# Optimization experiments

Measured on AMD Instinct MI355X. Metric: run time of the kernel, lower is better.

## Reference

```python
import jax, jax.numpy as jnp
import numpy as np

B, Q, V, H, U = 4, 256, 2048, 512, 128

def setup_inputs() -> dict:
    key = jax.random.key(0)
    ks = jax.random.split(key, 5)
    return {
        "queries": jax.random.normal(ks[0], (B, Q, H), dtype=jnp.float32),
        "values": jax.random.normal(ks[1], (B, V, H), dtype=jnp.float32),
        "w1": jax.random.normal(ks[2], (H, U), dtype=jnp.float32) / np.sqrt(H),
        "w2": jax.random.normal(ks[3], (H, U), dtype=jnp.float32) / np.sqrt(H),
        "v": jax.random.normal(ks[4], (U,), dtype=jnp.float32) / np.sqrt(U),
    }

def reference(queries, values, w1, w2, v):
    # Project queries and values first (cheap GEMMs), then broadcast-add.
    pq = jnp.einsum("bqh,hu->bqu", queries, w1)          # [B,Q,U]
    pv = jnp.einsum("bvh,hu->bvu", values, w2)           # [B,V,U]
    # added_qv: [B,Q,V,U] -- the large intermediate the original materializes
    scores = jnp.einsum("bqvu,u->bqv", jnp.tanh(pq[:, :, None, :] + pv[:, None, :, :]), v)
    attn = jax.nn.softmax(scores, axis=-1)               # softmax over V (last axis, as tf.nn.softmax)
    return jnp.einsum("bqv,bvh->bqh", attn, values)      # [B,Q,H]
```

## Files before the change

### kernel.cpp

```cpp
#include <hip/hip_runtime.h>

#define BB 4
#define QQ 256
#define VV 2048
#define HH 512
#define UU 128

#define C2E   2.8853900817779268f
#define LOG2E 1.4426950408889634f

__device__ __forceinline__ void fma4(float4& a, float s, const float4& w) {
    a.x = fmaf(s, w.x, a.x);
    a.y = fmaf(s, w.y, a.y);
    a.z = fmaf(s, w.z, a.z);
    a.w = fmaf(s, w.w, a.w);
}
__device__ __forceinline__ float2 rcp2(float2 x) {
    return make_float2(__builtin_amdgcn_rcpf(x.x), __builtin_amdgcn_rcpf(x.y));
}
__device__ __forceinline__ float2 mul2(float2 a, float2 b) { return make_float2(a.x*b.x, a.y*b.y); }
__device__ __forceinline__ float2 muls(float2 a, float s)  { return make_float2(a.x*s, a.y*s); }
__device__ __forceinline__ float2 fma2(float2 a, float2 b, float2 c) {
    return make_float2(fmaf(a.x, b.x, c.x), fmaf(a.y, b.y, c.y));
}
__device__ __forceinline__ float2 fmas(float2 a, float s, float2 c) {
    return make_float2(fmaf(a.x, s, c.x), fmaf(a.y, s, c.y));
}

__global__ __launch_bounds__(256) void proj_kernel(const float* __restrict__ queries,
                                                   const float* __restrict__ values,
                                                   const float* __restrict__ w1,
                                                   const float* __restrict__ w2,
                                                   float* __restrict__ pqI,
                                                   float* __restrict__ pvI,
                                                   float* __restrict__ denom) {
    __shared__ float As[32][18];
    __shared__ float Ws[32 * 128];
    __shared__ float Ls[128][17];
    const int bid = blockIdx.x;
    const int tid = threadIdx.x;
    if (bid == 0) *(float4*)&denom[tid * 4] = make_float4(0.f, 0.f, 0.f, 0.f);

    const bool isv = (bid < 512);
    const float* A; const float* W; int b, r0, ROWS; float* Ob;
    if (isv) {
        b = bid >> 7; r0 = (bid & 127) * 16;
        A = values + ((size_t)(b * VV + r0)) * HH;  W = w2;
        Ob = pvI + (size_t)b * UU * VV;  ROWS = VV;
    } else {
        const int q = bid - 512;
        b = q >> 4; r0 = (q & 15) * 16;
        A = queries + ((size_t)(b * QQ + r0)) * HH; W = w1;
        Ob = pqI + (size_t)b * UU * QQ;  ROWS = QQ;
    }

    const int tx = tid & 31;
    const int ty = tid >> 5;
    float4 acc0 = make_float4(0.f, 0.f, 0.f, 0.f);
    float4 acc1 = make_float4(0.f, 0.f, 0.f, 0.f);

    for (int k0 = 0; k0 < HH; k0 += 32) {
        if (tid < 128) {
            const int r = tid >> 3, kk4 = (tid & 7) * 4;
            const float4 a = *(const float4*)&A[(size_t)r * HH + k0 + kk4];
            As[kk4 + 0][r] = a.x; As[kk4 + 1][r] = a.y;
            As[kk4 + 2][r] = a.z; As[kk4 + 3][r] = a.w;
        }
#pragma unroll
        for (int t = 0; t < 4; t++) {
            const int f = tid + t * 256;
            const int kk = f >> 5, u4 = (f & 31) * 4;
            *(float4*)&Ws[kk * 128 + u4] = *(const float4*)&W[(size_t)(k0 + kk) * UU + u4];
        }
        __syncthreads();
#pragma unroll
        for (int kk = 0; kk < 32; kk++) {
            const float2 a = *(const float2*)&As[kk][ty * 2];
            const float4 w = *(const float4*)&Ws[kk * 128 + tx * 4];
            fma4(acc0, a.x, w);
            fma4(acc1, a.y, w);
        }
        __syncthreads();
    }
    {
        const float a0[4] = {acc0.x, acc0.y, acc0.z, acc0.w};
        const float a1[4] = {acc1.x, acc1.y, acc1.z, acc1.w};
#pragma unroll
        for (int i = 0; i < 4; i++) {
            Ls[tx * 4 + i][ty * 2 + 0] = __builtin_amdgcn_exp2f(a0[i] * C2E);
            Ls[tx * 4 + i][ty * 2 + 1] = __builtin_amdgcn_exp2f(a1[i] * C2E);
        }
    }
    __syncthreads();
#pragma unroll
    for (int t = 0; t < 2; t++) {
        const int idx = tid + t * 256;
        const int g = idx >> 4, r = idx & 15;
        float4 o;
        o.x = Ls[4 * g + 0][r]; o.y = Ls[4 * g + 1][r];
        o.z = Ls[4 * g + 2][r]; o.w = Ls[4 * g + 3][r];
        *(float4*)&Ob[((size_t)g * ROWS + r0 + r) * 4] = o;
    }
}

__global__ __launch_bounds__(512, 6) void fused_kernel(const float* __restrict__ pqI,
                                                       const float* __restrict__ pvI,
                                                       const float* __restrict__ vvec,
                                                       const float* __restrict__ values,
                                                       float* __restrict__ slab,
                                                       float* __restrict__ denom) {
    __shared__ float att[256][8];
    __shared__ float scratch[8][512];
    __shared__ float wred[4][8];
    const int tid = threadIdx.x;
    const int bid = blockIdx.x;
    const int vs = bid & 7, qb = (bid >> 3) & 31, b = bid >> 8;
    const int qbase = qb * 8, vbase = vs * 256;

    const int vloc = tid & 255, uh = tid >> 8;
    const int v = vbase + vloc;

    float vsum = 0.0f;
#pragma unroll
    for (int u4 = 0; u4 < UU; u4 += 4) {
        const float4 t = *(const float4*)&vvec[u4];
        vsum += t.x + t.y + t.z + t.w;
    }

    const float* pv4 = pvI + (size_t)b * UU * VV + (size_t)v * 4;
    const float* pq4 = pqI + (size_t)b * UU * QQ + (size_t)qbase * 4;

    float2 acc[4];
#pragma unroll
    for (int p = 0; p < 4; p++) acc[p] = make_float2(0.f, 0.f);

    const int G0 = uh * 16;
    float4 ev = *(const float4*)&pv4[(size_t)G0 * VV * 4];

    for (int g = 0; g < 16; g++) {
        const int G = G0 + g;
        const float* eqp = &pq4[(size_t)G * QQ * 4];
        float4 eq[8];
#pragma unroll
        for (int qi = 0; qi < 8; qi++) eq[qi] = *(const float4*)&eqp[qi * 4];
        float4 evn;
        if (g < 15) evn = *(const float4*)&pv4[(size_t)(G + 1) * VV * 4];
        const float4 wq = *(const float4*)&vvec[G * 4];
        const float w0 = 2.f * wq.x, w1 = 2.f * wq.y;
        const float w2 = 2.f * wq.z, w3 = 2.f * wq.w;
#pragma unroll
        for (int p = 0; p < 4; p++) {
            const float4 e0 = eq[2 * p], e1 = eq[2 * p + 1];
            const float2 a1 = make_float2(fmaf(e0.x, ev.x, 1.f), fmaf(e1.x, ev.x, 1.f));
            const float2 b1 = make_float2(fmaf(e0.y, ev.y, 1.f), fmaf(e1.y, ev.y, 1.f));
            const float2 c1 = make_float2(fmaf(e0.z, ev.z, 1.f), fmaf(e1.z, ev.z, 1.f));
            const float2 d1 = make_float2(fmaf(e0.w, ev.w, 1.f), fmaf(e1.w, ev.w, 1.f));
            const float2 pab = mul2(a1, b1), pcd = mul2(c1, d1);
            const float2 nab = fmas(a1, w1, muls(b1, w0));
            const float2 ncd = fmas(c1, w3, muls(d1, w2));
            const float2 num = fma2(nab, pcd, mul2(ncd, pab));
            const float2 den = mul2(pab, pcd);
            acc[p] = fma2(num, rcp2(den), acc[p]);
        }
        ev = evn;
    }

    float* cbuf = &scratch[0][0];
    if (uh == 1) {
#pragma unroll
        for (int p = 0; p < 4; p++)
            *(float2*)&cbuf[vloc * 8 + 2 * p] = acc[p];
    }
    __syncthreads();
    if (uh == 0) {
#pragma unroll
        for (int p = 0; p < 4; p++) {
            const float2 hi = *(const float2*)&cbuf[vloc * 8 + 2 * p];
            float2 e;
            e.x = __builtin_amdgcn_exp2f((vsum - (acc[p].x + hi.x)) * LOG2E);
            e.y = __builtin_amdgcn_exp2f((vsum - (acc[p].y + hi.y)) * LOG2E);
            att[vloc][2 * p + 0] = e.x;
            att[vloc][2 * p + 1] = e.y;
            acc[p] = e;
        }
#pragma unroll
        for (int off = 1; off < 64; off <<= 1) {
#pragma unroll
            for (int p = 0; p < 4; p++) {
                acc[p].x += __shfl_xor(acc[p].x, off, 64);
                acc[p].y += __shfl_xor(acc[p].y, off, 64);
            }
        }
        if ((tid & 63) == 0) {
            const int w = tid >> 6;
#pragma unroll
            for (int p = 0; p < 4; p++) {
                wred[w][2 * p + 0] = acc[p].x;
                wred[w][2 * p + 1] = acc[p].y;
            }
        }
    }
    __syncthreads();
    if (tid < 8)
        atomicAdd(&denom[b * QQ + qbase + tid],
                  wred[0][tid] + wred[1][tid] + wred[2][tid] + wred[3][tid]);

    const int hg = tid & 127, sel = tid >> 7;
    const int qh = sel & 1, vh = sel >> 1;
    const int h0 = hg * 4;
    const float* vp = values + ((size_t)(b * VV + vbase + vh * 128)) * HH + h0;

    float4 oacc[4];
#pragma unroll
    for (int j = 0; j < 4; j++) oacc[j] = make_float4(0.f, 0.f, 0.f, 0.f);

#pragma unroll 2
    for (int vv = 0; vv < 128; vv++) {
        const float4 w = *(const float4*)&vp[(size_t)vv * HH];
        const float4 a = *(const float4*)&att[vh * 128 + vv][qh * 4];
        fma4(oacc[0], a.x, w); fma4(oacc[1], a.y, w);
        fma4(oacc[2], a.z, w); fma4(oacc[3], a.w, w);
    }

    if (vh == 1) {
#pragma unroll
        for (int j = 0; j < 4; j++) *(float4*)&scratch[qh * 4 + j][h0] = oacc[j];
    }
    __syncthreads();
    if (vh == 0) {
        float* sp = slab + (size_t)vs * (BB * QQ * HH);
#pragma unroll
        for (int j = 0; j < 4; j++) {
            const float4 p4 = *(const float4*)&scratch[qh * 4 + j][h0];
            const int q = qh * 4 + j;
            float4 o;
            o.x = oacc[j].x + p4.x; o.y = oacc[j].y + p4.y;
            o.z = oacc[j].z + p4.z; o.w = oacc[j].w + p4.w;
            *(float4*)&sp[((size_t)(b * QQ + qbase + q)) * HH + h0] = o;
        }
    }
}

__global__ __launch_bounds__(256) void reduce_kernel(const float* __restrict__ slab,
                                                     const float* __restrict__ denom,
                                                     float* __restrict__ out) {
    const int i = blockIdx.x * 256 + threadIdx.x;
    const float r = __builtin_amdgcn_rcpf(denom[i >> 7]);
    const float4* s4 = (const float4*)slab;
    float4 s = s4[i];
#pragma unroll
    for (int k = 1; k < 8; k++) {
        const float4 p = s4[(size_t)k * (BB * QQ * HH / 4) + i];
        s.x += p.x; s.y += p.y; s.z += p.z; s.w += p.w;
    }
    s.x *= r; s.y *= r; s.z *= r; s.w *= r;
    ((float4*)out)[i] = s;
}

extern "C" void kernel_launch(void* const* d_in, const int* in_sizes, int n_in,
                              void* d_out, int out_size, void* d_ws, size_t ws_size,
                              hipStream_t stream) {
    const float* queries = (const float*)d_in[0];
    const float* values  = (const float*)d_in[1];
    const float* w1      = (const float*)d_in[2];
    const float* w2      = (const float*)d_in[3];
    const float* vvec    = (const float*)d_in[4];
    float* out = (float*)d_out;

    float* ws    = (float*)d_ws;
    float* pqI   = ws;
    float* pvI   = pqI + BB * UU * QQ;
    float* denom = pvI + (size_t)BB * UU * VV;
    float* slab  = denom + BB * QQ;

    proj_kernel<<<512 + 64, 256, 0, stream>>>(queries, values, w1, w2, pqI, pvI, denom);
    fused_kernel<<<BB * (QQ / 8) * (VV / 256), 512, 0, stream>>>(pqI, pvI, vvec, values, slab, denom);
    reduce_kernel<<<(BB * QQ * HH) / 4 / 256, 256, 0, stream>>>(slab, denom, out);
}
```

Before: 189.5 us.

## Double per-block query tile in fused and projection kernels for more reuse

The fused kernel now handles 16 queries per block instead of 8, so each pv element and each values row loaded in the attention-weighted sum is reused across twice as many queries, and the grid halves to 512 blocks. The projection kernel computes 32 rows per block with a 4x4 register tile and shares one LDS buffer between the A/W tiles and the transpose buffer. Register pressure in the fused kernel rises (8 float2 plus 8 float4 accumulators under a 512x6 launch bound), so spills or lower occupancy are a risk, and the smaller grid may leave some CUs less busy.

Measured after the change: 173.3 us. -8.5%, faster.

```diff
diff --git a/kernel.cpp b/kernel.cpp
--- a/kernel.cpp
+++ b/kernel.cpp
@@ -34,33 +34,36 @@
                                                    float* __restrict__ pqI,
                                                    float* __restrict__ pvI,
                                                    float* __restrict__ denom) {
-    __shared__ float As[32][18];
-    __shared__ float Ws[32 * 128];
-    __shared__ float Ls[128][17];
+    __shared__ float smem[32 * 36 + 32 * 128];
+    float (*As)[36] = (float(*)[36])smem;
+    float* Ws = smem + 32 * 36;
+    float (*Ls)[36] = (float(*)[36])smem;
+
     const int bid = blockIdx.x;
     const int tid = threadIdx.x;
     if (bid == 0) *(float4*)&denom[tid * 4] = make_float4(0.f, 0.f, 0.f, 0.f);
 
-    const bool isv = (bid < 512);
+    const bool isv = (bid < 256);
     const float* A; const float* W; int b, r0, ROWS; float* Ob;
     if (isv) {
-        b = bid >> 7; r0 = (bid & 127) * 16;
+        b = bid >> 6; r0 = (bid & 63) * 32;
         A = values + ((size_t)(b * VV + r0)) * HH;  W = w2;
         Ob = pvI + (size_t)b * UU * VV;  ROWS = VV;
     } else {
-        const int q = bid - 512;
-        b = q >> 4; r0 = (q & 15) * 16;
+        const int q = bid - 256;
+        b = q >> 3; r0 = (q & 7) * 32;
         A = queries + ((size_t)(b * QQ + r0)) * HH; W = w1;
         Ob = pqI + (size_t)b * UU * QQ;  ROWS = QQ;
     }
 
     const int tx = tid & 31;
     const int ty = tid >> 5;
-    float4 acc0 = make_float4(0.f, 0.f, 0.f, 0.f);
-    float4 acc1 = make_float4(0.f, 0.f, 0.f, 0.f);
+    float4 acc[4];
+#pragma unroll
+    for (int j = 0; j < 4; j++) acc[j] = make_float4(0.f, 0.f, 0.f, 0.f);
 
     for (int k0 = 0; k0 < HH; k0 += 32) {
-        if (tid < 128) {
+        {
             const int r = tid >> 3, kk4 = (tid & 7) * 4;
             const float4 a = *(const float4*)&A[(size_t)r * HH + k0 + kk4];
             As[kk4 + 0][r] = a.x; As[kk4 + 1][r] = a.y;
@@ -75,27 +78,27 @@
         __syncthreads();
 #pragma unroll
         for (int kk = 0; kk < 32; kk++) {
-            const float2 a = *(const float2*)&As[kk][ty * 2];
+            const float4 a = *(const float4*)&As[kk][ty * 4];
             const float4 w = *(const float4*)&Ws[kk * 128 + tx * 4];
-            fma4(acc0, a.x, w);
-            fma4(acc1, a.y, w);
+            fma4(acc[0], a.x, w);
+            fma4(acc[1], a.y, w);
+            fma4(acc[2], a.z, w);
+            fma4(acc[3], a.w, w);
         }
         __syncthreads();
     }
-    {
-        const float a0[4] = {acc0.x, acc0.y, acc0.z, acc0.w};
-        const float a1[4] = {acc1.x, acc1.y, acc1.z, acc1.w};
-#pragma unroll
-        for (int i = 0; i < 4; i++) {
-            Ls[tx * 4 + i][ty * 2 + 0] = __builtin_amdgcn_exp2f(a0[i] * C2E);
-            Ls[tx * 4 + i][ty * 2 + 1] = __builtin_amdgcn_exp2f(a1[i] * C2E);
-        }
-    }
-    __syncthreads();
-#pragma unroll
-    for (int t = 0; t < 2; t++) {
+#pragma unroll
+    for (int j = 0; j < 4; j++) {
+        const float aa[4] = {acc[j].x, acc[j].y, acc[j].z, acc[j].w};
+#pragma unroll
+        for (int i = 0; i < 4; i++)
+            Ls[tx * 4 + i][ty * 4 + j] = __builtin_amdgcn_exp2f(aa[i] * C2E);
+    }
+    __syncthreads();
+#pragma unroll
+    for (int t = 0; t < 4; t++) {
         const int idx = tid + t * 256;
-        const int g = idx >> 4, r = idx & 15;
+        const int g = idx >> 5, r = idx & 31;
         float4 o;
         o.x = Ls[4 * g + 0][r]; o.y = Ls[4 * g + 1][r];
         o.z = Ls[4 * g + 2][r]; o.w = Ls[4 * g + 3][r];
@@ -109,13 +112,13 @@
                                                        const float* __restrict__ values,
                                                        float* __restrict__ slab,
                                                        float* __restrict__ denom) {
-    __shared__ float att[256][8];
-    __shared__ float scratch[8][512];
-    __shared__ float wred[4][8];
+    __shared__ float att[256][16];
+    __shared__ float scratch[16][512];
+    __shared__ float wred[4][16];
     const int tid = threadIdx.x;
     const int bid = blockIdx.x;
-    const int vs = bid & 7, qb = (bid >> 3) & 31, b = bid >> 8;
-    const int qbase = qb * 8, vbase = vs * 256;
+    const int vs = bid & 7, qb = (bid >> 3) & 15, b = bid >> 7;
+    const int qbase = qb * 16, vbase = vs * 256;
 
     const int vloc = tid & 255, uh = tid >> 8;
     const int v = vbase + vloc;
@@ -130,9 +133,9 @@
     const float* pv4 = pvI + (size_t)b * UU * VV + (size_t)v * 4;
     const float* pq4 = pqI + (size_t)b * UU * QQ + (size_t)qbase * 4;
 
-    float2 acc[4];
-#pragma unroll
-    for (int p = 0; p < 4; p++) acc[p] = make_float2(0.f, 0.f);
+    float2 acc[8];
+#pragma unroll
+    for (int p = 0; p < 8; p++) acc[p] = make_float2(0.f, 0.f);
 
     const int G0 = uh * 16;
     float4 ev = *(const float4*)&pv4[(size_t)G0 * VV * 4];
@@ -140,17 +143,15 @@
     for (int g = 0; g < 16; g++) {
         const int G = G0 + g;
         const float* eqp = &pq4[(size_t)G * QQ * 4];
-        float4 eq[8];
-#pragma unroll
-        for (int qi = 0; qi < 8; qi++) eq[qi] = *(const float4*)&eqp[qi * 4];
         float4 evn;
         if (g < 15) evn = *(const float4*)&pv4[(size_t)(G + 1) * VV * 4];
         const float4 wq = *(const float4*)&vvec[G * 4];
         const float w0 = 2.f * wq.x, w1 = 2.f * wq.y;
         const float w2 = 2.f * wq.z, w3 = 2.f * wq.w;
 #pragma unroll
-        for (int p = 0; p < 4; p++) {
-            const float4 e0 = eq[2 * p], e1 = eq[2 * p + 1];
+        for (int p = 0; p < 8; p++) {
+            const float4 e0 = *(const float4*)&eqp[(2 * p) * 4];
+            const float4 e1 = *(const float4*)&eqp[(2 * p + 1) * 4];
             const float2 a1 = make_float2(fmaf(e0.x, ev.x, 1.f), fmaf(e1.x, ev.x, 1.f));
             const float2 b1 = make_float2(fmaf(e0.y, ev.y, 1.f), fmaf(e1.y, ev.y, 1.f));
             const float2 c1 = make_float2(fmaf(e0.z, ev.z, 1.f), fmaf(e1.z, ev.z, 1.f));
@@ -168,14 +169,14 @@
     float* cbuf = &scratch[0][0];
     if (uh == 1) {
 #pragma unroll
-        for (int p = 0; p < 4; p++)
-            *(float2*)&cbuf[vloc * 8 + 2 * p] = acc[p];
+        for (int p = 0; p < 8; p++)
+            *(float2*)&cbuf[vloc * 16 + 2 * p] = acc[p];
     }
     __syncthreads();
     if (uh == 0) {
 #pragma unroll
-        for (int p = 0; p < 4; p++) {
-            const float2 hi = *(const float2*)&cbuf[vloc * 8 + 2 * p];
+        for (int p = 0; p < 8; p++) {
+            const float2 hi = *(const float2*)&cbuf[vloc * 16 + 2 * p];
             float2 e;
             e.x = __builtin_amdgcn_exp2f((vsum - (acc[p].x + hi.x)) * LOG2E);
             e.y = __builtin_amdgcn_exp2f((vsum - (acc[p].y + hi.y)) * LOG2E);
@@ -186,7 +187,7 @@
 #pragma unroll
         for (int off = 1; off < 64; off <<= 1) {
 #pragma unroll
-            for (int p = 0; p < 4; p++) {
+            for (int p = 0; p < 8; p++) {
                 acc[p].x += __shfl_xor(acc[p].x, off, 64);
                 acc[p].y += __shfl_xor(acc[p].y, off, 64);
             }
@@ -194,14 +195,14 @@
         if ((tid & 63) == 0) {
             const int w = tid >> 6;
 #pragma unroll
-            for (int p = 0; p < 4; p++) {
+            for (int p = 0; p < 8; p++) {
                 wred[w][2 * p + 0] = acc[p].x;
                 wred[w][2 * p + 1] = acc[p].y;
             }
         }
     }
     __syncthreads();
-    if (tid < 8)
+    if (tid < 16)
         atomicAdd(&denom[b * QQ + qbase + tid],
                   wred[0][tid] + wred[1][tid] + wred[2][tid] + wred[3][tid]);
 
@@ -210,29 +211,32 @@
     const int h0 = hg * 4;
     const float* vp = values + ((size_t)(b * VV + vbase + vh * 128)) * HH + h0;
 
-    float4 oacc[4];
-#pragma unroll
-    for (int j = 0; j < 4; j++) oacc[j] = make_float4(0.f, 0.f, 0.f, 0.f);
+    float4 oacc[8];
+#pragma unroll
+    for (int j = 0; j < 8; j++) oacc[j] = make_float4(0.f, 0.f, 0.f, 0.f);
 
 #pragma unroll 2
     for (int vv = 0; vv < 128; vv++) {
         const float4 w = *(const float4*)&vp[(size_t)vv * HH];
-        const float4 a = *(const float4*)&att[vh * 128 + vv][qh * 4];
-        fma4(oacc[0], a.x, w); fma4(oacc[1], a.y, w);
-        fma4(oacc[2], a.z, w); fma4(oacc[3], a.w, w);
+        const float4 a0 = *(const float4*)&att[vh * 128 + vv][qh * 8 + 0];
+        const float4 a1 = *(const float4*)&att[vh * 128 + vv][qh * 8 + 4];
+        fma4(oacc[0], a0.x, w); fma4(oacc[1], a0.y, w);
+        fma4(oacc[2], a0.z, w); fma4(oacc[3], a0.w, w);
+        fma4(oacc[4], a1.x, w); fma4(oacc[5], a1.y, w);
+        fma4(oacc[6], a1.z, w); fma4(oacc[7], a1.w, w);
     }
 
     if (vh == 1) {
 #pragma unroll
-        for (int j = 0; j < 4; j++) *(float4*)&scratch[qh * 4 + j][h0] = oacc[j];
+        for (int j = 0; j < 8; j++) *(float4*)&scratch[qh * 8 + j][h0] = oacc[j];
     }
     __syncthreads();
     if (vh == 0) {
         float* sp = slab + (size_t)vs * (BB * QQ * HH);
 #pragma unroll
-        for (int j = 0; j < 4; j++) {
-            const float4 p4 = *(const float4*)&scratch[qh * 4 + j][h0];
-            const int q = qh * 4 + j;
+        for (int j = 0; j < 8; j++) {
+            const float4 p4 = *(const float4*)&scratch[qh * 8 + j][h0];
+            const int q = qh * 8 + j;
             float4 o;
             o.x = oacc[j].x + p4.x; o.y = oacc[j].y + p4.y;
             o.z = oacc[j].z + p4.z; o.w = oacc[j].w + p4.w;
@@ -273,7 +277,7 @@
     float* denom = pvI + (size_t)BB * UU * VV;
     float* slab  = denom + BB * QQ;
 
-    proj_kernel<<<512 + 64, 256, 0, stream>>>(queries, values, w1, w2, pqI, pvI, denom);
-    fused_kernel<<<BB * (QQ / 8) * (VV / 256), 512, 0, stream>>>(pqI, pvI, vvec, values, slab, denom);
+    proj_kernel<<<256 + 32, 256, 0, stream>>>(queries, values, w1, w2, pqI, pvI, denom);
+    fused_kernel<<<BB * (QQ / 16) * (VV / 256), 512, 0, stream>>>(pqI, pvI, vvec, values, slab, denom);
     reduce_kernel<<<(BB * QQ * HH) / 4 / 256, 256, 0, stream>>>(slab, denom, out);
 }
```
